# Kernel optimization log

Measured on AMD Instinct MI355X. Metric: run time of the kernel, lower is better.

Reference implementation:

```python
import jax, jax.numpy as jnp
import numpy as np

S = 8          # num_slots
DSLOT = 128    # slot_dim
D_IN = 768     # input feature dim
ITERS = 3      # slot_att_iter
RES = 21       # 336 // 16
NGRID = RES * RES   # 441 grid positions
NTOK = 441          # tokens kept per frame (no drop here)
NFRAME = 2
F_ = 2 * NFRAME + 1  # 5 frames per clip
CLIPS = 8
B = CLIPS * F_       # 40
SIGMA = 5.0
SCALE = DSLOT ** -0.5
EPS = 1e-8


def layernorm(x, g, b):
    m = x.mean(-1, keepdims=True)
    v = ((x - m) ** 2).mean(-1, keepdims=True)
    return (x - m) * jax.lax.rsqrt(v + 1e-5) * g + b


def setup_inputs() -> dict:
    key = jax.random.key(0)
    ks = iter(jax.random.split(key, 64))
    def nrm(shape, s=0.02):
        return jax.random.normal(next(ks), shape, jnp.float32) * s
    xs = jnp.linspace(-1.0, 1.0, RES)
    ys = jnp.linspace(-1.0, 1.0, RES)
    gx, gy = jnp.meshgrid(xs, ys)  # indexing='xy' as in torch
    abs_grid = jnp.stack([gx.ravel(), gy.ravel()], axis=-1)  # [NGRID, 2]
    return {
        "inputs": jax.random.normal(next(ks), (B, NTOK, D_IN), jnp.float32),
        "token_indices": jnp.sort(jax.random.randint(next(ks), (B, NTOK), 0, NGRID), axis=-1),
        "abs_grid": abs_grid,
        "slots_init": nrm((1, S, DSLOT), 0.1),
        "S_p_init": nrm((1, S, 1, 2), 0.02),
        "S_s_init": jax.random.uniform(next(ks), (1, S, 1, 2), jnp.float32, 0.3, 0.7),
        "WQ": nrm((DSLOT, DSLOT)), "ln_g": jnp.ones((DSLOT,)), "ln_b": jnp.zeros((DSLOT,)),
        "gru_w_ih": nrm((DSLOT, 3 * DSLOT)), "gru_w_hh": nrm((DSLOT, 3 * DSLOT)),
        "gru_b_ih": jnp.zeros((3 * DSLOT,)), "gru_b_hh": jnp.zeros((3 * DSLOT,)),
        "mlp_ln_g": jnp.ones((DSLOT,)), "mlp_ln_b": jnp.zeros((DSLOT,)),
        "mlp_w1": nrm((DSLOT, 4 * DSLOT)), "mlp_b1": jnp.zeros((4 * DSLOT,)),
        "mlp_w2": nrm((4 * DSLOT, DSLOT)), "mlp_b2": jnp.zeros((DSLOT,)),
        "WK": nrm((DSLOT, DSLOT)), "WV": nrm((DSLOT, DSLOT)),
        "Wg": nrm((2, DSLOT)), "bg": jnp.zeros((DSLOT,)),
        "Wf1": nrm((DSLOT, DSLOT)), "bf1": jnp.zeros((DSLOT,)),
        "Wf2": nrm((DSLOT, DSLOT)), "bf2": jnp.zeros((DSLOT,)),
        "im_ln1_g": jnp.ones((D_IN,)), "im_ln1_b": jnp.zeros((D_IN,)),
        "im_w1": nrm((D_IN, D_IN)), "im_b1": jnp.zeros((D_IN,)),
        "im_w2": nrm((D_IN, DSLOT)), "im_b2": jnp.zeros((DSLOT,)),
        "im_ln2_g": jnp.ones((DSLOT,)), "im_ln2_b": jnp.zeros((DSLOT,)),
        "fin_w": nrm((DSLOT, DSLOT)), "fin_b": jnp.zeros((DSLOT,)),
    }


def _forward(inputs, token_indices, abs_grid, slots_init, S_p_init, S_s_init,
             WQ, ln_g, ln_b, gru_w_ih, gru_w_hh, gru_b_ih, gru_b_hh,
             mlp_ln_g, mlp_ln_b, mlp_w1, mlp_b1, mlp_w2, mlp_b2,
             WK, WV, Wg, bg, Wf1, bf1, Wf2, bf2,
             im_ln1_g, im_ln1_b, im_w1, im_b1, im_w2, im_b2, im_ln2_g, im_ln2_b,
             fin_w, fin_b):
    Bb = inputs.shape[0]
    # initial_mlp: LN -> Linear -> ReLU -> Linear -> LN
    x = layernorm(inputs, im_ln1_g, im_ln1_b)
    x = jax.nn.relu(x @ im_w1 + im_b1)
    x = x @ im_w2 + im_b2
    x = layernorm(x, im_ln2_g, im_ln2_b)          # [B, N, Dslot]
    # K/V projections of inputs are slot-independent; compute once.
    Kx = x @ WK                                    # [B, N, Dslot]
    Vx = x @ WV
    ag = abs_grid[token_indices]                   # [B, N, 2] per-batch gather
    slots = jnp.broadcast_to(slots_init, (Bb, S, DSLOT))
    S_p = jnp.broadcast_to(S_p_init, (Bb, S, 1, 2))
    S_s = jnp.broadcast_to(S_s_init, (Bb, S, 1, 2))

    def f_net(z):  # f = Linear -> ReLU -> Linear
        return jax.nn.relu(z @ Wf1 + bf1) @ Wf2 + bf2

    attn = None
    for t in range(ITERS + 1):
        slots_prev = slots
        sn = layernorm(slots, ln_g, ln_b)
        rel = (ag[:, None] - S_p) / (S_s * SIGMA)  # [B, S, N, 2]
        gr = rel @ Wg + bg                          # [B, S, N, Dslot]
        k = f_net(Kx[:, None] + gr)
        v = f_net(Vx[:, None] + gr)
        q = sn @ WQ                                 # [B, S, Dslot]
        dots = jnp.einsum('bsd,bsjd->bsj', q, k) * SCALE
        attn = jax.nn.softmax(dots, axis=1) + EPS   # softmax over slots
        attn = attn / attn.sum(-1, keepdims=True)   # renormalize over tokens
        updates = jnp.einsum('bsjd,bsj->bsd', v, attn)
        S_p = jnp.einsum('bjd,bsj->bsd', ag, attn)[:, :, None, :]
        S_s = jnp.sqrt(jnp.einsum('bsjd,bsj->bsd', (ag[:, None] - S_p) ** 2, attn))[:, :, None, :]
        if t != ITERS:
            # torch GRUCell
            xg = updates.reshape(-1, DSLOT)
            hg = slots_prev.reshape(-1, DSLOT)
            gi = xg @ gru_w_ih + gru_b_ih
            gh = hg @ gru_w_hh + gru_b_hh
            i_r, i_z, i_n = jnp.split(gi, 3, axis=-1)
            h_r, h_z, h_n = jnp.split(gh, 3, axis=-1)
            r = jax.nn.sigmoid(i_r + h_r)
            z = jax.nn.sigmoid(i_z + h_z)
            n = jnp.tanh(i_n + r * h_n)
            slots = ((1.0 - z) * n + z * hg).reshape(Bb, S, DSLOT)
            # residual pre-LN MLP (dropout is identity in eval)
            y = layernorm(slots, mlp_ln_g, mlp_ln_b)
            y = jax.nn.relu(y @ mlp_w1 + mlp_b1) @ mlp_w2 + mlp_b2
            slots = slots + y
    slots = slots @ fin_w + fin_b
    attn_out = attn.reshape(-1, F_, S, NTOK)[:, NFRAME]  # center frame
    return slots, attn_out


def reference(inputs, token_indices, abs_grid, slots_init, S_p_init, S_s_init,
              WQ, ln_g, ln_b, gru_w_ih, gru_w_hh, gru_b_ih, gru_b_hh,
              mlp_ln_g, mlp_ln_b, mlp_w1, mlp_b1, mlp_w2, mlp_b2,
              WK, WV, Wg, bg, Wf1, bf1, Wf2, bf2,
              im_ln1_g, im_ln1_b, im_w1, im_b1, im_w2, im_b2, im_ln2_g, im_ln2_b,
              fin_w, fin_b):
    return _forward(inputs, token_indices, abs_grid, slots_init, S_p_init, S_s_init,
                    WQ, ln_g, ln_b, gru_w_ih, gru_w_hh, gru_b_ih, gru_b_hh,
                    mlp_ln_g, mlp_ln_b, mlp_w1, mlp_b1, mlp_w2, mlp_b2,
                    WK, WV, Wg, bg, Wf1, bf1, Wf2, bf2,
                    im_ln1_g, im_ln1_b, im_w1, im_b1, im_w2, im_b2, im_ln2_g, im_ln2_b,
                    fin_w, fin_b)
```

## Files before the change

### kernel.cpp

```cpp
#include <hip/hip_runtime.h>
#include <cstdio>

#define NB 40
#define NS 8
#define NT 441
#define DIN 768
#define DD 128
#define NTOT (NB*NT)
#define FSCALE 0.08838834764831843f

typedef short s8v __attribute__((ext_vector_type(8)));
typedef float f4v __attribute__((ext_vector_type(4)));

__device__ inline ushort f2bf(float f){
  unsigned u = __float_as_uint(f);
  unsigned r = (u + 0x7fffu + ((u >> 16) & 1u)) >> 16;
  return (ushort)r;
}
__device__ inline float bf2f(ushort h){ return __uint_as_float(((unsigned)h) << 16); }

struct PP {
  const float *inputs; const int *tok_idx; const float *abs_grid;
  const float *slots_init, *Sp_init, *Ss_init;
  const float *WQ, *ln_g, *ln_b;
  const float *gru_w_ih, *gru_w_hh, *gru_b_ih, *gru_b_hh;
  const float *mlp_ln_g, *mlp_ln_b, *mlp_w1, *mlp_b1, *mlp_w2, *mlp_b2;
  const float *WK, *WV, *Wg, *bg, *Wf1, *bf1, *Wf2, *bf2;
  const float *im_ln1_g, *im_ln1_b, *im_w1, *im_b1, *im_w2, *im_b2, *im_ln2_g, *im_ln2_b;
  const float *fin_w, *fin_b;
  float *A_K, *A_V, *Wg1, *c1, *Wf2T;
  float *slots_g, *qw_g, *qb_g, *spss_g, *hpart_g, *a_g;
  ushort *xnh, *xnl, *hh, *hl, *W1Th, *W1Tl, *W2Th, *W2Tl;
  ushort *WKfTh, *WKfTl, *WVfTh, *WVfTl;
  float *out;
};

__global__ __launch_bounds__(128) void prep_weights(PP p){
  int r = blockIdx.x, d = threadIdx.x;
  float accK = 0.f, accV = 0.f;
  for (int kk = 0; kk < DD; kk++){
    float w = p.Wf1[kk*DD + d];
    accK = fmaf(p.WK[r*DD+kk], w, accK);
    accV = fmaf(p.WV[r*DD+kk], w, accV);
  }
  ushort hk = f2bf(accK), hv = f2bf(accV);
  p.WKfTh[d*DD + r] = hk; p.WKfTl[d*DD + r] = f2bf(accK - bf2f(hk));
  p.WVfTh[d*DD + r] = hv; p.WVfTl[d*DD + r] = f2bf(accV - bf2f(hv));
  if (r < 2){
    float a = 0.f;
    for (int kk = 0; kk < DD; kk++) a = fmaf(p.Wg[r*DD+kk], p.Wf1[kk*DD+d], a);
    p.Wg1[r*DD+d] = a;
  }
  if (r == 2){
    float a = 0.f;
    for (int kk = 0; kk < DD; kk++) a = fmaf(p.bg[kk], p.Wf1[kk*DD+d], a);
    p.c1[d] = a + p.bf1[d];
  }
  p.Wf2T[d*DD + r] = p.Wf2[r*DD + d];
}

__global__ __launch_bounds__(256) void transpose_both(PP p){
  __shared__ float tile[64][65];
  int t = blockIdx.x;
  const float* W; ushort *WTh, *WTl; int N, k0, n0;
  if (t < 144){ W = p.im_w1; WTh = p.W1Th; WTl = p.W1Tl; N = 768; k0 = (t/12)*64; n0 = (t%12)*64; }
  else { t -= 144; W = p.im_w2; WTh = p.W2Th; WTl = p.W2Tl; N = 128; k0 = (t/2)*64; n0 = (t&1)*64; }
  int tid = threadIdx.x;
  #pragma unroll
  for (int i = 0; i < 4; i++){
    int k = i*16 + (tid >> 4);
    int n4 = (tid & 15) * 4;
    float4 v = *(const float4*)(W + (long)(k0+k)*N + n0 + n4);
    tile[k][n4+0] = v.x; tile[k][n4+1] = v.y; tile[k][n4+2] = v.z; tile[k][n4+3] = v.w;
  }
  __syncthreads();
  #pragma unroll
  for (int i = 0; i < 4; i++){
    int n = i*16 + (tid >> 4);
    int k4 = (tid & 15) * 4;
    ushort4 h4, l4;
    float v0 = tile[k4+0][n], v1 = tile[k4+1][n], v2 = tile[k4+2][n], v3 = tile[k4+3][n];
    h4.x = f2bf(v0); l4.x = f2bf(v0 - bf2f(h4.x));
    h4.y = f2bf(v1); l4.y = f2bf(v1 - bf2f(h4.y));
    h4.z = f2bf(v2); l4.z = f2bf(v2 - bf2f(h4.z));
    h4.w = f2bf(v3); l4.w = f2bf(v3 - bf2f(h4.w));
    *(ushort4*)(WTh + (long)(n0+n)*DIN + k0 + k4) = h4;
    *(ushort4*)(WTl + (long)(n0+n)*DIN + k0 + k4) = l4;
  }
}

__device__ void phase0g(const PP& p, int bs, int tid, float* scr, const float* sl,
                        float Sp0, float Sp1, float Ss0, float Ss1){
  float* sn   = scr;
  float* qv   = scr + 128;
  float* part = scr + 256;
  float* red  = scr + 512;
  int o = tid & 127, h = tid >> 7;
  float v = (tid < 128) ? sl[tid] : 0.f;
  float s1 = v, s2 = v*v;
  #pragma unroll
  for (int m = 1; m < 64; m <<= 1){ s1 += __shfl_xor(s1,m); s2 += __shfl_xor(s2,m); }
  if (tid < 128 && (tid & 63) == 0){ red[(tid>>6)*2] = s1; red[(tid>>6)*2+1] = s2; }
  __syncthreads();
  float mean = (red[0]+red[2])*(1.f/128.f);
  float var  = (red[1]+red[3])*(1.f/128.f) - mean*mean;
  float rstd = rsqrtf(var + 1e-5f);
  if (tid < 128) sn[tid] = (v-mean)*rstd*p.ln_g[tid] + p.ln_b[tid];
  __syncthreads();
  float acc = 0.f;
  for (int k = 0; k < 64; k++) acc = fmaf(sn[h*64+k], p.WQ[(h*64+k)*128+o], acc);
  part[h*128+o] = acc;
  __syncthreads();
  if (tid < 128) qv[tid] = part[tid] + part[128+tid];
  __syncthreads();
  float acc2 = 0.f;
  for (int k = 0; k < 64; k++) acc2 = fmaf(qv[h*64+k], p.Wf2T[(h*64+k)*128+o], acc2);
  part[h*128+o] = acc2;
  __syncthreads();
  if (tid < 128) p.qw_g[(long)bs*128+tid] = part[tid] + part[128+tid];
  float pb = (tid < 128) ? qv[tid]*p.bf2[tid] : 0.f;
  #pragma unroll
  for (int m = 1; m < 64; m <<= 1) pb += __shfl_xor(pb,m);
  if ((tid & 63) == 0) red[4 + (tid>>6)] = pb;
  __syncthreads();
  if (tid == 0){
    p.qb_g[bs] = FSCALE*(red[4]+red[5]+red[6]+red[7]);
    p.spss_g[bs*4+0] = Sp0; p.spss_g[bs*4+1] = Sp1;
    p.spss_g[bs*4+2] = 1.f/(Ss0*5.0f); p.spss_g[bs*4+3] = 1.f/(Ss1*5.0f);
  }
}

__global__ __launch_bounds__(256) void ln1_init(PP p){
  __shared__ float sl[128];
  __shared__ float scr[520];
  if (blockIdx.x < 4410){
    int tok = blockIdx.x*4 + (threadIdx.x >> 6);
    int l = threadIdx.x & 63;
    const float* src = p.inputs + (long)tok*DIN;
    float4 v[3];
    float s = 0.f, s2 = 0.f;
    #pragma unroll
    for (int pp = 0; pp < 3; pp++){
      v[pp] = *(const float4*)(src + pp*256 + l*4);
      s  += v[pp].x + v[pp].y + v[pp].z + v[pp].w;
      s2 += v[pp].x*v[pp].x + v[pp].y*v[pp].y + v[pp].z*v[pp].z + v[pp].w*v[pp].w;
    }
    #pragma unroll
    for (int m = 1; m < 64; m <<= 1){ s += __shfl_xor(s, m); s2 += __shfl_xor(s2, m); }
    float mean = s*(1.f/DIN), var = s2*(1.f/DIN) - mean*mean;
    float rstd = rsqrtf(var + 1e-5f);
    #pragma unroll
    for (int pp = 0; pp < 3; pp++){
      int idx = pp*256 + l*4;
      float4 g = *(const float4*)(p.im_ln1_g + idx);
      float4 b = *(const float4*)(p.im_ln1_b + idx);
      float y0 = (v[pp].x-mean)*rstd*g.x + b.x;
      float y1 = (v[pp].y-mean)*rstd*g.y + b.y;
      float y2 = (v[pp].z-mean)*rstd*g.z + b.z;
      float y3 = (v[pp].w-mean)*rstd*g.w + b.w;
      ushort4 h4, l4;
      h4.x = f2bf(y0); l4.x = f2bf(y0 - bf2f(h4.x));
      h4.y = f2bf(y1); l4.y = f2bf(y1 - bf2f(h4.y));
      h4.z = f2bf(y2); l4.z = f2bf(y2 - bf2f(h4.z));
      h4.w = f2bf(y3); l4.w = f2bf(y3 - bf2f(h4.w));
      *(ushort4*)(p.xnh + (long)tok*DIN + idx) = h4;
      *(ushort4*)(p.xnl + (long)tok*DIN + idx) = l4;
    }
  } else {
    int bs = blockIdx.x - 4410, ss = bs & 7, tid = threadIdx.x;
    if (tid < 128){
      float v = p.slots_init[ss*128+tid];
      sl[tid] = v;
      p.slots_g[(long)bs*128+tid] = v;
    }
    __syncthreads();
    phase0g(p, bs, tid, scr, sl,
            p.Sp_init[ss*2], p.Sp_init[ss*2+1], p.Ss_init[ss*2], p.Ss_init[ss*2+1]);
  }
}

__global__ __launch_bounds__(256) void gemm1_128(PP p){
  __shared__ __align__(16) ushort As[2][128][40];
  __shared__ __align__(16) ushort Bs[2][128][40];
  int id = blockIdx.x;
  int xcd = id & 7, idx = id >> 3;
  int m_t = xcd + 8*(idx/6), n_t = idx % 6;
  if (m_t >= 138) return;
  int m0 = m_t*128, n0 = n_t*128;
  int tid = threadIdx.x;
  int w = tid >> 6, lane = tid & 63;
  int wm = w >> 1, wn = w & 1;
  f4v acc[4][4];
  #pragma unroll
  for (int mf = 0; mf < 4; mf++)
    #pragma unroll
    for (int nf = 0; nf < 4; nf++) acc[mf][nf] = (f4v)(0.f);

  for (int kb = 0; kb < DIN; kb += 32){
    __syncthreads();
    #pragma unroll
    for (int i = 0; i < 4; i++){
      int c = tid + i*256;
      int s = c >> 9, rem = c & 511;
      int r = rem >> 2, kg = rem & 3;
      int gr = min(m0 + r, NTOT-1);
      const float4 va = *(const float4*)((s ? p.xnl : p.xnh) + (long)gr*DIN + kb + kg*8);
      *(float4*)(&As[s][r][kg*8]) = va;
      const float4 vb = *(const float4*)((s ? p.W1Tl : p.W1Th) + (long)(n0 + r)*DIN + kb + kg*8);
      *(float4*)(&Bs[s][r][kg*8]) = vb;
    }
    __syncthreads();
    int kg = lane >> 4, rA = lane & 15;
    s8v a0[4], a1[4], b0[4], b1[4];
    #pragma unroll
    for (int mf = 0; mf < 4; mf++){
      a0[mf] = *(const s8v*)(&As[0][wm*64 + mf*16 + rA][kg*8]);
      a1[mf] = *(const s8v*)(&As[1][wm*64 + mf*16 + rA][kg*8]);
    }
    #pragma unroll
    for (int nf = 0; nf < 4; nf++){
      b0[nf] = *(const s8v*)(&Bs[0][wn*64 + nf*16 + rA][kg*8]);
      b1[nf] = *(const s8v*)(&Bs[1][wn*64 + nf*16 + rA][kg*8]);
    }
    #pragma unroll
    for (int mf = 0; mf < 4; mf++)
      #pragma unroll
      for (int nf = 0; nf < 4; nf++){
        acc[mf][nf] = __builtin_amdgcn_mfma_f32_16x16x32_bf16(a0[mf], b0[nf], acc[mf][nf], 0, 0, 0);
        acc[mf][nf] = __builtin_amdgcn_mfma_f32_16x16x32_bf16(a0[mf], b1[nf], acc[mf][nf], 0, 0, 0);
        acc[mf][nf] = __builtin_amdgcn_mfma_f32_16x16x32_bf16(a1[mf], b0[nf], acc[mf][nf], 0, 0, 0);
      }
  }

  int rbase = (lane >> 4) * 4, cn = lane & 15;
  #pragma unroll
  for (int mf = 0; mf < 4; mf++)
    #pragma unroll
    for (int nf = 0; nf < 4; nf++){
      int n = n0 + wn*64 + nf*16 + cn;
      float bs = p.im_b1[n];
      #pragma unroll
      for (int r = 0; r < 4; r++){
        int m = m0 + wm*64 + mf*16 + rbase + r;
        if (m < NTOT){
          float v = fmaxf(acc[mf][nf][r] + bs, 0.f);
          ushort h = f2bf(v);
          p.hh[(long)m*DIN + n] = h;
          p.hl[(long)m*DIN + n] = f2bf(v - bf2f(h));
        }
      }
    }
}

__global__ __launch_bounds__(256) void gemm2_fused(PP p){
  extern __shared__ __align__(16) char smem[];
  ushort* As = (ushort*)smem;
  ushort* Bs = (ushort*)(smem + 10240);
  float*  Dl = (float*)smem;
  ushort* xsh = (ushort*)(smem + 33792);
  ushort* xsl = (ushort*)(smem + 33792 + 17408);
  int m0 = blockIdx.x * 64;
  int tid = threadIdx.x, w = tid >> 6, lane = tid & 63;
  f4v acc[4][2];
  #pragma unroll
  for (int mf = 0; mf < 4; mf++)
    #pragma unroll
    for (int nf = 0; nf < 2; nf++) acc[mf][nf] = (f4v)(0.f);

  for (int kb = 0; kb < DIN; kb += 32){
    __syncthreads();
    #pragma unroll
    for (int i = 0; i < 2; i++){
      int c = tid + i*256;
      int s = c >> 8, r = (c >> 2) & 63, kg = c & 3;
      int gr = min(m0 + r, NTOT-1);
      const float4 va = *(const float4*)((s ? p.hl : p.hh) + (long)gr*DIN + kb + kg*8);
      *(float4*)(As + s*2560 + r*40 + kg*8) = va;
    }
    #pragma unroll
    for (int i = 0; i < 4; i++){
      int c = tid + i*256;
      int s = c >> 9, r = (c >> 2) & 127, kg = c & 3;
      const float4 vb = *(const float4*)((s ? p.W2Tl : p.W2Th) + (long)r*DIN + kb + kg*8);
      *(float4*)(Bs + s*5120 + r*40 + kg*8) = vb;
    }
    __syncthreads();
    int kg = lane >> 4, rA = lane & 15;
    s8v a0[4], a1[4], b0[2], b1[2];
    #pragma unroll
    for (int mf = 0; mf < 4; mf++){
      a0[mf] = *(const s8v*)(As +        (mf*16 + rA)*40 + kg*8);
      a1[mf] = *(const s8v*)(As + 2560 + (mf*16 + rA)*40 + kg*8);
    }
    #pragma unroll
    for (int nf = 0; nf < 2; nf++){
      int rb = w*32 + nf*16 + rA;
      b0[nf] = *(const s8v*)(Bs +        rb*40 + kg*8);
      b1[nf] = *(const s8v*)(Bs + 5120 + rb*40 + kg*8);
    }
    #pragma unroll
    for (int mf = 0; mf < 4; mf++)
      #pragma unroll
      for (int nf = 0; nf < 2; nf++){
        acc[mf][nf] = __builtin_amdgcn_mfma_f32_16x16x32_bf16(a0[mf], b0[nf], acc[mf][nf], 0, 0, 0);
        acc[mf][nf] = __builtin_amdgcn_mfma_f32_16x16x32_bf16(a0[mf], b1[nf], acc[mf][nf], 0, 0, 0);
        acc[mf][nf] = __builtin_amdgcn_mfma_f32_16x16x32_bf16(a1[mf], b0[nf], acc[mf][nf], 0, 0, 0);
      }
  }

  int rbase = (lane >> 4) * 4, cn = lane & 15;
  __syncthreads();
  #pragma unroll
  for (int mf = 0; mf < 4; mf++)
    #pragma unroll
    for (int nf = 0; nf < 2; nf++){
      int n = w*32 + nf*16 + cn;
      float bs = p.im_b2[n];
      #pragma unroll
      for (int r = 0; r < 4; r++)
        Dl[(mf*16 + rbase + r)*132 + n] = acc[mf][nf][r] + bs;
    }
  __syncthreads();
  for (int rr = 0; rr < 16; rr++){
    int row = w*16 + rr;
    float e0 = Dl[row*132 + lane], e1 = Dl[row*132 + 64 + lane];
    float s = e0 + e1, s2 = e0*e0 + e1*e1;
    #pragma unroll
    for (int m2 = 1; m2 < 64; m2 <<= 1){ s += __shfl_xor(s, m2); s2 += __shfl_xor(s2, m2); }
    float mean = s*(1.f/DD), var = s2*(1.f/DD) - mean*mean;
    float rstd = rsqrtf(var + 1e-5f);
    float x0 = (e0-mean)*rstd*p.im_ln2_g[lane]    + p.im_ln2_b[lane];
    float x1 = (e1-mean)*rstd*p.im_ln2_g[64+lane] + p.im_ln2_b[64+lane];
    ushort h0 = f2bf(x0), h1 = f2bf(x1);
    xsh[row*136 + lane]      = h0;  xsl[row*136 + lane]      = f2bf(x0 - bf2f(h0));
    xsh[row*136 + 64 + lane] = h1;  xsl[row*136 + 64 + lane] = f2bf(x1 - bf2f(h1));
  }
  __syncthreads();
  int kg = lane >> 4, rA = lane & 15;
  f4v aK[8], aV[8];
  #pragma unroll
  for (int nf = 0; nf < 8; nf++){ aK[nf] = (f4v)(0.f); aV[nf] = (f4v)(0.f); }
  #pragma unroll
  for (int kb2 = 0; kb2 < 4; kb2++){
    s8v ah = *(const s8v*)&xsh[(w*16+rA)*136 + kb2*32 + kg*8];
    s8v al = *(const s8v*)&xsl[(w*16+rA)*136 + kb2*32 + kg*8];
    #pragma unroll
    for (int nf = 0; nf < 8; nf++){
      int n = nf*16 + rA;
      s8v bh = *(const s8v*)(p.WKfTh + n*DD + kb2*32 + kg*8);
      s8v bl = *(const s8v*)(p.WKfTl + n*DD + kb2*32 + kg*8);
      aK[nf] = __builtin_amdgcn_mfma_f32_16x16x32_bf16(ah, bh, aK[nf], 0, 0, 0);
      aK[nf] = __builtin_amdgcn_mfma_f32_16x16x32_bf16(ah, bl, aK[nf], 0, 0, 0);
      aK[nf] = __builtin_amdgcn_mfma_f32_16x16x32_bf16(al, bh, aK[nf], 0, 0, 0);
      s8v ch = *(const s8v*)(p.WVfTh + n*DD + kb2*32 + kg*8);
      s8v cl = *(const s8v*)(p.WVfTl + n*DD + kb2*32 + kg*8);
      aV[nf] = __builtin_amdgcn_mfma_f32_16x16x32_bf16(ah, ch, aV[nf], 0, 0, 0);
      aV[nf] = __builtin_amdgcn_mfma_f32_16x16x32_bf16(ah, cl, aV[nf], 0, 0, 0);
      aV[nf] = __builtin_amdgcn_mfma_f32_16x16x32_bf16(al, ch, aV[nf], 0, 0, 0);
    }
  }
  #pragma unroll
  for (int nf = 0; nf < 8; nf++){
    int n = nf*16 + cn;
    float c = p.c1[n];
    #pragma unroll
    for (int r = 0; r < 4; r++){
      int m = m0 + w*16 + rbase + r;
      if (m < NTOT){
        p.A_K[(long)m*DD + n] = aK[nf][r] + c;
        p.A_V[(long)m*DD + n] = aV[nf][r] + c;
      }
    }
  }
}

template<int LAST>
__global__ __launch_bounds__(256) void kA(PP p){
  int b = blockIdx.x / 7, tile = blockIdx.x % 7;
  int tid = threadIdx.x, wid = tid >> 6, lane = tid & 63;
  __shared__ float qws[8][132];
  __shared__ float qbs[8];
  __shared__ float spssL[32];
  __shared__ float agt[64][2];
  __shared__ float a_tile[8][64];
  __shared__ float hpartL[4][8][128];
  for (int f = tid; f < 8*128; f += 256){
    int s = f >> 7, d = f & 127;
    qws[s][(d&31)*4 + (d>>5)] = p.qw_g[((long)b*8+s)*128 + d];
  }
  if (tid < 8)  qbs[tid] = p.qb_g[b*8+tid];
  if (tid < 32) spssL[tid] = p.spss_g[b*32+tid];
  if (tid < 64){
    int j = tile*64 + tid;
    float g0 = 0.f, g1 = 0.f;
    if (j < NT){ int idx = p.tok_idx[b*NT+j]; g0 = p.abs_grid[idx*2]; g1 = p.abs_grid[idx*2+1]; }
    agt[tid][0] = g0; agt[tid][1] = g1;
  }
  __syncthreads();

  {
    int tl = lane >> 2, dg = lane & 3;
    int jtok = wid*16 + tl, j = tile*64 + jtok;
    bool valid = j < NT;
    int jc = valid ? j : 0;
    float aa[32], w0[32], w1[32];
    const float* src = p.A_K + ((long)(b*NT+jc))*DD + dg*32;
    #pragma unroll
    for (int i4 = 0; i4 < 8; i4++){
      float4 t = *(const float4*)(src + i4*4);
      aa[i4*4+0]=t.x; aa[i4*4+1]=t.y; aa[i4*4+2]=t.z; aa[i4*4+3]=t.w;
    }
    #pragma unroll
    for (int i4 = 0; i4 < 8; i4++){
      float4 t0 = *(const float4*)(p.Wg1 + dg*32 + i4*4);
      float4 t1 = *(const float4*)(p.Wg1 + DD + dg*32 + i4*4);
      w0[i4*4+0]=t0.x; w0[i4*4+1]=t0.y; w0[i4*4+2]=t0.z; w0[i4*4+3]=t0.w;
      w1[i4*4+0]=t1.x; w1[i4*4+1]=t1.y; w1[i4*4+2]=t1.z; w1[i4*4+3]=t1.w;
    }
    float ag0 = agt[jtok][0], ag1 = agt[jtok][1];
    float dv[8];
    #pragma unroll
    for (int s = 0; s < 8; s++){
      float rel0 = (ag0 - spssL[s*4+0])*spssL[s*4+2];
      float rel1 = (ag1 - spssL[s*4+1])*spssL[s*4+3];
      float acc = 0.f;
      #pragma unroll
      for (int i = 0; i < 32; i++){
        float hk = fmaxf(fmaf(rel0, w0[i], fmaf(rel1, w1[i], aa[i])), 0.f);
        acc = fmaf(hk, qws[s][i*4+dg], acc);
      }
      acc += __shfl_xor(acc, 1); acc += __shfl_xor(acc, 2);
      dv[s] = acc*FSCALE + qbs[s];
    }
    if (dg == 0){
      float m = -1e30f;
      #pragma unroll
      for (int s = 0; s < 8; s++) m = fmaxf(m, dv[s]);
      float tot = 0.f;
      #pragma unroll
      for (int s = 0; s < 8; s++){ dv[s] = expf(dv[s]-m); tot += dv[s]; }
      float inv = 1.f/tot;
      #pragma unroll
      for (int s = 0; s < 8; s++)
        a_tile[s][jtok] = valid ? (dv[s]*inv + 1e-8f) : 0.f;
    }
  }
  __syncthreads();

  #pragma unroll
  for (int si = 0; si < 2; si++){
    int s = wid*2 + si;
    float a = a_tile[s][lane];
    float g0 = agt[lane][0], g1 = agt[lane][1];
    float v0 = a, v1 = a*g0, v2 = a*g1, v3 = a*g0*g0, v4 = a*g1*g1;
    #pragma unroll
    for (int m = 1; m < 64; m <<= 1){
      v0 += __shfl_xor(v0,m); v1 += __shfl_xor(v1,m); v2 += __shfl_xor(v2,m);
      v3 += __shfl_xor(v3,m); v4 += __shfl_xor(v4,m);
    }
    if (lane == 0){
      float* st = p.hpart_g + ((long)(b*7+tile)*8 + s)*136 + 128;
      st[0]=v0; st[1]=v1; st[2]=v2; st[3]=v3; st[4]=v4;
    }
  }

  if (LAST){
    if ((b % 5) == 2){
      int clip = b/5;
      for (int f = tid; f < 8*64; f += 256){
        int s = f >> 6, jt = f & 63;
        int j = tile*64 + jt;
        if (j < NT) p.a_g[((long)clip*8 + s)*NT + j] = a_tile[s][jt];
      }
    }
    return;
  }

  {
    float sp0[8], sp1[8], si0[8], si1[8];
    #pragma unroll
    for (int s = 0; s < 8; s++){
      sp0[s]=spssL[s*4+0]; sp1[s]=spssL[s*4+1]; si0[s]=spssL[s*4+2]; si1[s]=spssL[s*4+3];
    }
    int d0 = lane, d1 = lane + 64;
    float wg0a = p.Wg1[d0], wg1a = p.Wg1[DD+d0];
    float wg0b = p.Wg1[d1], wg1b = p.Wg1[DD+d1];
    float acc0[8], acc1[8];
    #pragma unroll
    for (int s = 0; s < 8; s++){ acc0[s]=0.f; acc1[s]=0.f; }
    for (int jj = wid; jj < 64; jj += 4){
      int j = tile*64 + jj;
      if (j >= NT) continue;
      float av0 = p.A_V[((long)(b*NT+j))*DD + d0];
      float av1 = p.A_V[((long)(b*NT+j))*DD + d1];
      float g0 = agt[jj][0], g1 = agt[jj][1];
      #pragma unroll
      for (int s = 0; s < 8; s++){
        float rel0 = (g0 - sp0[s])*si0[s];
        float rel1 = (g1 - sp1[s])*si1[s];
        float a = a_tile[s][jj];
        float hv0 = fmaxf(fmaf(rel0, wg0a, fmaf(rel1, wg1a, av0)), 0.f);
        float hv1 = fmaxf(fmaf(rel0, wg0b, fmaf(rel1, wg1b, av1)), 0.f);
        acc0[s] = fmaf(a, hv0, acc0[s]);
        acc1[s] = fmaf(a, hv1, acc1[s]);
      }
    }
    #pragma unroll
    for (int s = 0; s < 8; s++){ hpartL[wid][s][d0] = acc0[s]; hpartL[wid][s][d1] = acc1[s]; }
    __syncthreads();
    for (int f = tid; f < 1024; f += 256){
      int s = f >> 7, d = f & 127;
      p.hpart_g[((long)(b*7+tile)*8 + s)*136 + d] =
        hpartL[0][s][d] + hpartL[1][s][d] + hpartL[2][s][d] + hpartL[3][s][d];
    }
  }
}

template<int LAST>
__global__ __launch_bounds__(256) void kB(PP p){
  __shared__ float red[8];
  __shared__ float sl[128];
  __shared__ float hb[128];
  __shared__ float scr[2304];
  int bs = blockIdx.x, b = bs >> 3, ss = bs & 7, tid = threadIdx.x;
  if (tid < 5){
    float v = 0.f;
    #pragma unroll
    for (int t7 = 0; t7 < 7; t7++) v += p.hpart_g[((long)(b*7+t7)*8 + ss)*136 + 128 + tid];
    red[tid] = v;
  }
  __syncthreads();
  float SA = red[0], inv = 1.f/SA;
  float Sp0 = red[1]*inv, Sp1 = red[2]*inv;
  float Ss0 = sqrtf(fmaxf(red[3]*inv - Sp0*Sp0, 0.f));
  float Ss1 = sqrtf(fmaxf(red[4]*inv - Sp1*Sp1, 0.f));

  if (LAST){
    if ((b % 5) == 2){
      int clip = b/5;
      long base = (long)NB*NS*DD + ((long)clip*8 + ss)*NT;
      const float* arow = p.a_g + ((long)clip*8 + ss)*NT;
      for (int j = tid; j < NT; j += 256) p.out[base+j] = arow[j]*inv;
    }
    if (tid < 128) sl[tid] = p.slots_g[(long)bs*128+tid];
    __syncthreads();
    int o = tid & 127, h = tid >> 7;
    float acc = 0.f;
    for (int k = 0; k < 64; k++) acc = fmaf(sl[h*64+k], p.fin_w[(h*64+k)*128+o], acc);
    scr[h*128+o] = acc;
    __syncthreads();
    if (tid < 128) p.out[(long)bs*128+tid] = p.fin_b[tid] + scr[tid] + scr[128+tid];
    return;
  }

  if (tid < 128){
    float v = 0.f;
    #pragma unroll
    for (int t7 = 0; t7 < 7; t7++) v += p.hpart_g[((long)(b*7+t7)*8 + ss)*136 + tid];
    hb[tid] = v * inv;
    sl[tid] = p.slots_g[(long)bs*128+tid];
  }
  __syncthreads();
  float* part = scr;
  float* upd  = scr + 256;
  float* gil  = scr + 384;
  float* ghl  = scr + 768;
  float* hnl  = scr + 1152;
  float* yv   = scr + 1280;
  float* h1   = scr + 1408;
  int o = tid & 127, h = tid >> 7;
  float acc2 = 0.f;
  for (int k = 0; k < 64; k++) acc2 = fmaf(hb[h*64+k], p.Wf2[(h*64+k)*128+o], acc2);
  part[h*128+o] = acc2;
  __syncthreads();
  if (tid < 128) upd[tid] = part[tid] + part[128+tid] + p.bf2[tid];
  __syncthreads();
  int oA = tid, oB = tid + 256;
  float giA = p.gru_b_ih[oA], ghA = p.gru_b_hh[oA];
  float giB = 0.f, ghB = 0.f;
  if (tid < 128){ giB = p.gru_b_ih[oB]; ghB = p.gru_b_hh[oB]; }
  for (int k = 0; k < 128; k++){
    float uk = upd[k], sk = sl[k];
    giA = fmaf(uk, p.gru_w_ih[k*384+oA], giA);
    ghA = fmaf(sk, p.gru_w_hh[k*384+oA], ghA);
    if (tid < 128){
      giB = fmaf(uk, p.gru_w_ih[k*384+oB], giB);
      ghB = fmaf(sk, p.gru_w_hh[k*384+oB], ghB);
    }
  }
  gil[oA] = giA; ghl[oA] = ghA;
  if (tid < 128){ gil[oB] = giB; ghl[oB] = ghB; }
  __syncthreads();
  float hnv = 0.f;
  if (tid < 128){
    float r = 1.f/(1.f+expf(-(gil[tid]+ghl[tid])));
    float z = 1.f/(1.f+expf(-(gil[128+tid]+ghl[128+tid])));
    float n = tanhf(gil[256+tid] + r*ghl[256+tid]);
    hnv = (1.f-z)*n + z*sl[tid];
  }
  float t1 = hnv, t2 = hnv*hnv;
  #pragma unroll
  for (int m = 1; m < 64; m <<= 1){ t1 += __shfl_xor(t1,m); t2 += __shfl_xor(t2,m); }
  if (tid < 128 && (tid & 63) == 0){ red[(tid>>6)*2] = t1; red[(tid>>6)*2+1] = t2; }
  __syncthreads();
  float mean = (red[0]+red[2])*(1.f/128.f);
  float var  = (red[1]+red[3])*(1.f/128.f) - mean*mean;
  float rstd = rsqrtf(var + 1e-5f);
  if (tid < 128){
    hnl[tid] = hnv;
    yv[tid] = (hnv-mean)*rstd*p.mlp_ln_g[tid] + p.mlp_ln_b[tid];
  }
  __syncthreads();
  float m1A = p.mlp_b1[tid], m1B = p.mlp_b1[tid+256];
  for (int k = 0; k < 128; k++){
    float y = yv[k];
    m1A = fmaf(y, p.mlp_w1[k*512+tid], m1A);
    m1B = fmaf(y, p.mlp_w1[k*512+tid+256], m1B);
  }
  h1[tid] = fmaxf(m1A, 0.f); h1[tid+256] = fmaxf(m1B, 0.f);
  __syncthreads();
  float a2 = 0.f;
  for (int kk = 0; kk < 256; kk++) a2 = fmaf(h1[h*256+kk], p.mlp_w2[(h*256+kk)*128+o], a2);
  part[h*128+o] = a2;
  __syncthreads();
  if (tid < 128){
    float sln = hnl[tid] + p.mlp_b2[tid] + part[tid] + part[128+tid];
    sl[tid] = sln;
    p.slots_g[(long)bs*128+tid] = sln;
  }
  __syncthreads();
  phase0g(p, bs, tid, scr, sl, Sp0, Sp1, Ss0, Ss1);
}

extern "C" void kernel_launch(void* const* d_in, const int* in_sizes, int n_in,
                              void* d_out, int out_size, void* d_ws, size_t ws_size,
                              hipStream_t stream){
  PP p;
  p.inputs=(const float*)d_in[0]; p.tok_idx=(const int*)d_in[1]; p.abs_grid=(const float*)d_in[2];
  p.slots_init=(const float*)d_in[3]; p.Sp_init=(const float*)d_in[4]; p.Ss_init=(const float*)d_in[5];
  p.WQ=(const float*)d_in[6]; p.ln_g=(const float*)d_in[7]; p.ln_b=(const float*)d_in[8];
  p.gru_w_ih=(const float*)d_in[9]; p.gru_w_hh=(const float*)d_in[10];
  p.gru_b_ih=(const float*)d_in[11]; p.gru_b_hh=(const float*)d_in[12];
  p.mlp_ln_g=(const float*)d_in[13]; p.mlp_ln_b=(const float*)d_in[14];
  p.mlp_w1=(const float*)d_in[15]; p.mlp_b1=(const float*)d_in[16];
  p.mlp_w2=(const float*)d_in[17]; p.mlp_b2=(const float*)d_in[18];
  p.WK=(const float*)d_in[19]; p.WV=(const float*)d_in[20]; p.Wg=(const float*)d_in[21]; p.bg=(const float*)d_in[22];
  p.Wf1=(const float*)d_in[23]; p.bf1=(const float*)d_in[24]; p.Wf2=(const float*)d_in[25]; p.bf2=(const float*)d_in[26];
  p.im_ln1_g=(const float*)d_in[27]; p.im_ln1_b=(const float*)d_in[28];
  p.im_w1=(const float*)d_in[29]; p.im_b1=(const float*)d_in[30];
  p.im_w2=(const float*)d_in[31]; p.im_b2=(const float*)d_in[32];
  p.im_ln2_g=(const float*)d_in[33]; p.im_ln2_b=(const float*)d_in[34];
  p.fin_w=(const float*)d_in[35]; p.fin_b=(const float*)d_in[36];

  float* w = (float*)d_ws;
  size_t need = 0;
  auto alloc = [&](size_t nfl){ nfl = (nfl + 3) & ~(size_t)3; float* r = w + need; need += nfl; return r; };
  p.A_K  = alloc((size_t)NTOT*DD);
  p.A_V  = alloc((size_t)NTOT*DD);
  p.Wg1  = alloc(2*DD);
  p.c1   = alloc(DD);
  p.Wf2T = alloc(DD*DD);
  p.slots_g = alloc(320*128);
  p.qw_g    = alloc(320*128);
  p.qb_g    = alloc(320);
  p.spss_g  = alloc(320*4);
  p.hpart_g = alloc((size_t)280*8*136);
  p.a_g     = alloc((size_t)8*8*NT);
  p.xnh  = (ushort*)alloc((size_t)NTOT*DIN/2);
  p.xnl  = (ushort*)alloc((size_t)NTOT*DIN/2);
  p.hh   = (ushort*)alloc((size_t)NTOT*DIN/2);
  p.hl   = (ushort*)alloc((size_t)NTOT*DIN/2);
  p.W1Th = (ushort*)alloc((size_t)DIN*DIN/2);
  p.W1Tl = (ushort*)alloc((size_t)DIN*DIN/2);
  p.W2Th = (ushort*)alloc((size_t)DD*DIN/2);
  p.W2Tl = (ushort*)alloc((size_t)DD*DIN/2);
  p.WKfTh = (ushort*)alloc(DD*DD/2);
  p.WKfTl = (ushort*)alloc(DD*DD/2);
  p.WVfTh = (ushort*)alloc(DD*DD/2);
  p.WVfTl = (ushort*)alloc(DD*DD/2);
  p.out = (float*)d_out;
  if (ws_size < need*sizeof(float)){
    fprintf(stderr, "kernel_launch: ws too small (%zu < %zu)\n", ws_size, need*sizeof(float));
    return;
  }

  prep_weights<<<dim3(DD), dim3(128), 0, stream>>>(p);
  transpose_both<<<dim3(168), dim3(256), 0, stream>>>(p);
  ln1_init<<<dim3(4730), dim3(256), 0, stream>>>(p);
  gemm1_128<<<dim3(832), dim3(256), 0, stream>>>(p);
  gemm2_fused<<<dim3((NTOT+63)/64), dim3(256), 68608, stream>>>(p);

  for (int t = 0; t < 3; t++){
    kA<0><<<dim3(NB*7), dim3(256), 0, stream>>>(p);
    kB<0><<<dim3(320), dim3(256), 0, stream>>>(p);
  }
  kA<1><<<dim3(NB*7), dim3(256), 0, stream>>>(p);
  kB<1><<<dim3(320), dim3(256), 0, stream>>>(p);
}
```

Baseline: 438.2 us.

## Split attention kernel into 32-token tiles and pad GEMM shared-memory rows

The attention-logit kernel kA now covers 32 tokens per block instead of 64, giving 14 tiles per frame and twice as many blocks. Each token's 128-dim dot product is split across 8 lanes instead of 4, which halves per-thread registers and needs one extra shuffle step. kB sums twice as many partial results. Separately, the GEMM shared-memory row stride goes from 40 to 44 elements in both GEMM kernels to reduce LDS bank conflicts. The costs are more partial-sum traffic and half-idle lanes in the moment reduction.

```diff
diff --git a/kernel.cpp b/kernel.cpp
--- a/kernel.cpp
+++ b/kernel.cpp
@@ -7,6 +7,7 @@
 #define DIN 768
 #define DD 128
 #define NTOT (NB*NT)
+#define NTILE 14
 #define FSCALE 0.08838834764831843f
 
 typedef short s8v __attribute__((ext_vector_type(8)));
@@ -180,8 +181,8 @@
 }
 
 __global__ __launch_bounds__(256) void gemm1_128(PP p){
-  __shared__ __align__(16) ushort As[2][128][40];
-  __shared__ __align__(16) ushort Bs[2][128][40];
+  __shared__ __align__(16) ushort As[2][128][44];
+  __shared__ __align__(16) ushort Bs[2][128][44];
   int id = blockIdx.x;
   int xcd = id & 7, idx = id >> 3;
   int m_t = xcd + 8*(idx/6), n_t = idx % 6;
@@ -255,7 +256,7 @@
 __global__ __launch_bounds__(256) void gemm2_fused(PP p){
   extern __shared__ __align__(16) char smem[];
   ushort* As = (ushort*)smem;
-  ushort* Bs = (ushort*)(smem + 10240);
+  ushort* Bs = (ushort*)(smem + 11264);
   float*  Dl = (float*)smem;
   ushort* xsh = (ushort*)(smem + 33792);
   ushort* xsl = (ushort*)(smem + 33792 + 17408);
@@ -275,28 +276,28 @@
       int s = c >> 8, r = (c >> 2) & 63, kg = c & 3;
       int gr = min(m0 + r, NTOT-1);
       const float4 va = *(const float4*)((s ? p.hl : p.hh) + (long)gr*DIN + kb + kg*8);
-      *(float4*)(As + s*2560 + r*40 + kg*8) = va;
+      *(float4*)(As + s*2816 + r*44 + kg*8) = va;
     }
     #pragma unroll
     for (int i = 0; i < 4; i++){
       int c = tid + i*256;
       int s = c >> 9, r = (c >> 2) & 127, kg = c & 3;
       const float4 vb = *(const float4*)((s ? p.W2Tl : p.W2Th) + (long)r*DIN + kb + kg*8);
-      *(float4*)(Bs + s*5120 + r*40 + kg*8) = vb;
+      *(float4*)(Bs + s*5632 + r*44 + kg*8) = vb;
     }
     __syncthreads();
     int kg = lane >> 4, rA = lane & 15;
     s8v a0[4], a1[4], b0[2], b1[2];
     #pragma unroll
     for (int mf = 0; mf < 4; mf++){
-      a0[mf] = *(const s8v*)(As +        (mf*16 + rA)*40 + kg*8);
-      a1[mf] = *(const s8v*)(As + 2560 + (mf*16 + rA)*40 + kg*8);
+      a0[mf] = *(const s8v*)(As +        (mf*16 + rA)*44 + kg*8);
+      a1[mf] = *(const s8v*)(As + 2816 + (mf*16 + rA)*44 + kg*8);
     }
     #pragma unroll
     for (int nf = 0; nf < 2; nf++){
       int rb = w*32 + nf*16 + rA;
-      b0[nf] = *(const s8v*)(Bs +        rb*40 + kg*8);
-      b1[nf] = *(const s8v*)(Bs + 5120 + rb*40 + kg*8);
+      b0[nf] = *(const s8v*)(Bs +        rb*44 + kg*8);
+      b1[nf] = *(const s8v*)(Bs + 5632 + rb*44 + kg*8);
     }
     #pragma unroll
     for (int mf = 0; mf < 4; mf++)
@@ -376,22 +377,22 @@
 
 template<int LAST>
 __global__ __launch_bounds__(256) void kA(PP p){
-  int b = blockIdx.x / 7, tile = blockIdx.x % 7;
+  int b = blockIdx.x / NTILE, tile = blockIdx.x % NTILE;
   int tid = threadIdx.x, wid = tid >> 6, lane = tid & 63;
-  __shared__ float qws[8][132];
+  __shared__ float qws[8][128];
   __shared__ float qbs[8];
   __shared__ float spssL[32];
-  __shared__ float agt[64][2];
-  __shared__ float a_tile[8][64];
+  __shared__ float agt[32][2];
+  __shared__ float a_tile[8][32];
   __shared__ float hpartL[4][8][128];
   for (int f = tid; f < 8*128; f += 256){
     int s = f >> 7, d = f & 127;
-    qws[s][(d&31)*4 + (d>>5)] = p.qw_g[((long)b*8+s)*128 + d];
+    qws[s][(d&15)*8 + (d>>4)] = p.qw_g[((long)b*8+s)*128 + d];
   }
   if (tid < 8)  qbs[tid] = p.qb_g[b*8+tid];
   if (tid < 32) spssL[tid] = p.spss_g[b*32+tid];
-  if (tid < 64){
-    int j = tile*64 + tid;
+  if (tid < 32){
+    int j = tile*32 + tid;
     float g0 = 0.f, g1 = 0.f;
     if (j < NT){ int idx = p.tok_idx[b*NT+j]; g0 = p.abs_grid[idx*2]; g1 = p.abs_grid[idx*2+1]; }
     agt[tid][0] = g0; agt[tid][1] = g1;
@@ -399,25 +400,20 @@
   __syncthreads();
 
   {
-    int tl = lane >> 2, dg = lane & 3;
-    int jtok = wid*16 + tl, j = tile*64 + jtok;
+    int dg = tid & 7, jl = tid >> 3;
+    int j = tile*32 + jl;
     bool valid = j < NT;
     int jc = valid ? j : 0;
-    float aa[32], w0[32], w1[32];
-    const float* src = p.A_K + ((long)(b*NT+jc))*DD + dg*32;
-    #pragma unroll
-    for (int i4 = 0; i4 < 8; i4++){
+    float aa[16], w0[16], w1[16];
+    const float* src = p.A_K + ((long)(b*NT+jc))*DD + dg*16;
+    #pragma unroll
+    for (int i4 = 0; i4 < 4; i4++){
       float4 t = *(const float4*)(src + i4*4);
       aa[i4*4+0]=t.x; aa[i4*4+1]=t.y; aa[i4*4+2]=t.z; aa[i4*4+3]=t.w;
     }
     #pragma unroll
-    for (int i4 = 0; i4 < 8; i4++){
-      float4 t0 = *(const float4*)(p.Wg1 + dg*32 + i4*4);
-      float4 t1 = *(const float4*)(p.Wg1 + DD + dg*32 + i4*4);
-      w0[i4*4+0]=t0.x; w0[i4*4+1]=t0.y; w0[i4*4+2]=t0.z; w0[i4*4+3]=t0.w;
-      w1[i4*4+0]=t1.x; w1[i4*4+1]=t1.y; w1[i4*4+2]=t1.z; w1[i4*4+3]=t1.w;
-    }
-    float ag0 = agt[jtok][0], ag1 = agt[jtok][1];
+    for (int i = 0; i < 16; i++){ w0[i] = p.Wg1[dg*16+i]; w1[i] = p.Wg1[DD + dg*16+i]; }
+    float ag0 = agt[jl][0], ag1 = agt[jl][1];
     float dv[8];
     #pragma unroll
     for (int s = 0; s < 8; s++){
@@ -425,11 +421,11 @@
       float rel1 = (ag1 - spssL[s*4+1])*spssL[s*4+3];
       float acc = 0.f;
       #pragma unroll
-      for (int i = 0; i < 32; i++){
+      for (int i = 0; i < 16; i++){
         float hk = fmaxf(fmaf(rel0, w0[i], fmaf(rel1, w1[i], aa[i])), 0.f);
-        acc = fmaf(hk, qws[s][i*4+dg], acc);
+        acc = fmaf(hk, qws[s][i*8+dg], acc);
       }
-      acc += __shfl_xor(acc, 1); acc += __shfl_xor(acc, 2);
+      acc += __shfl_xor(acc, 1); acc += __shfl_xor(acc, 2); acc += __shfl_xor(acc, 4);
       dv[s] = acc*FSCALE + qbs[s];
     }
     if (dg == 0){
@@ -442,7 +438,7 @@
       float inv = 1.f/tot;
       #pragma unroll
       for (int s = 0; s < 8; s++)
-        a_tile[s][jtok] = valid ? (dv[s]*inv + 1e-8f) : 0.f;
+        a_tile[s][jl] = valid ? (dv[s]*inv + 1e-8f) : 0.f;
     }
   }
   __syncthreads();
@@ -450,8 +446,10 @@
   #pragma unroll
   for (int si = 0; si < 2; si++){
     int s = wid*2 + si;
-    float a = a_tile[s][lane];
-    float g0 = agt[lane][0], g1 = agt[lane][1];
+    bool tv = lane < 32;
+    float a = tv ? a_tile[s][lane & 31] : 0.f;
+    float g0 = tv ? agt[lane & 31][0] : 0.f;
+    float g1 = tv ? agt[lane & 31][1] : 0.f;
     float v0 = a, v1 = a*g0, v2 = a*g1, v3 = a*g0*g0, v4 = a*g1*g1;
     #pragma unroll
     for (int m = 1; m < 64; m <<= 1){
@@ -459,7 +457,7 @@
       v3 += __shfl_xor(v3,m); v4 += __shfl_xor(v4,m);
     }
     if (lane == 0){
-      float* st = p.hpart_g + ((long)(b*7+tile)*8 + s)*136 + 128;
+      float* st = p.hpart_g + ((long)(b*NTILE+tile)*8 + s)*136 + 128;
       st[0]=v0; st[1]=v1; st[2]=v2; st[3]=v3; st[4]=v4;
     }
   }
@@ -467,9 +465,9 @@
   if (LAST){
     if ((b % 5) == 2){
       int clip = b/5;
-      for (int f = tid; f < 8*64; f += 256){
-        int s = f >> 6, jt = f & 63;
-        int j = tile*64 + jt;
+      for (int f = tid; f < 8*32; f += 256){
+        int s = f >> 5, jt = f & 31;
+        int j = tile*32 + jt;
         if (j < NT) p.a_g[((long)clip*8 + s)*NT + j] = a_tile[s][jt];
       }
     }
@@ -488,8 +486,8 @@
     float acc0[8], acc1[8];
     #pragma unroll
     for (int s = 0; s < 8; s++){ acc0[s]=0.f; acc1[s]=0.f; }
-    for (int jj = wid; jj < 64; jj += 4){
-      int j = tile*64 + jj;
+    for (int jj = wid; jj < 32; jj += 4){
+      int j = tile*32 + jj;
       if (j >= NT) continue;
       float av0 = p.A_V[((long)(b*NT+j))*DD + d0];
       float av1 = p.A_V[((long)(b*NT+j))*DD + d1];
@@ -510,7 +508,7 @@
     __syncthreads();
     for (int f = tid; f < 1024; f += 256){
       int s = f >> 7, d = f & 127;
-      p.hpart_g[((long)(b*7+tile)*8 + s)*136 + d] =
+      p.hpart_g[((long)(b*NTILE+tile)*8 + s)*136 + d] =
         hpartL[0][s][d] + hpartL[1][s][d] + hpartL[2][s][d] + hpartL[3][s][d];
     }
   }
@@ -526,7 +524,7 @@
   if (tid < 5){
     float v = 0.f;
     #pragma unroll
-    for (int t7 = 0; t7 < 7; t7++) v += p.hpart_g[((long)(b*7+t7)*8 + ss)*136 + 128 + tid];
+    for (int t7 = 0; t7 < NTILE; t7++) v += p.hpart_g[((long)(b*NTILE+t7)*8 + ss)*136 + 128 + tid];
     red[tid] = v;
   }
   __syncthreads();
@@ -556,7 +554,7 @@
   if (tid < 128){
     float v = 0.f;
     #pragma unroll
-    for (int t7 = 0; t7 < 7; t7++) v += p.hpart_g[((long)(b*7+t7)*8 + ss)*136 + tid];
+    for (int t7 = 0; t7 < NTILE; t7++) v += p.hpart_g[((long)(b*NTILE+t7)*8 + ss)*136 + tid];
     hb[tid] = v * inv;
     sl[tid] = p.slots_g[(long)bs*128+tid];
   }
@@ -664,7 +662,7 @@
   p.qw_g    = alloc(320*128);
   p.qb_g    = alloc(320);
   p.spss_g  = alloc(320*4);
-  p.hpart_g = alloc((size_t)280*8*136);
+  p.hpart_g = alloc((size_t)NB*NTILE*8*136);
   p.a_g     = alloc((size_t)8*8*NT);
   p.xnh  = (ushort*)alloc((size_t)NTOT*DIN/2);
   p.xnl  = (ushort*)alloc((size_t)NTOT*DIN/2);
@@ -691,9 +689,9 @@
   gemm2_fused<<<dim3((NTOT+63)/64), dim3(256), 68608, stream>>>(p);
 
   for (int t = 0; t < 3; t++){
-    kA<0><<<dim3(NB*7), dim3(256), 0, stream>>>(p);
+    kA<0><<<dim3(NB*NTILE), dim3(256), 0, stream>>>(p);
     kB<0><<<dim3(320), dim3(256), 0, stream>>>(p);
   }
-  kA<1><<<dim3(NB*7), dim3(256), 0, stream>>>(p);
+  kA<1><<<dim3(NB*NTILE), dim3(256), 0, stream>>>(p);
   kB<1><<<dim3(320), dim3(256), 0, stream>>>(p);
 }
```

New measurement: 496.9 us. 13.4% more time.
